# Optimization experiments

Measured on AMD Instinct MI355X. Metric: run time of the kernel, lower is better.

The kernel has to match this reference:

```python
import jax, jax.numpy as jnp
import numpy as np

B, P, F, D = 1024, 128, 512, 256
THETA = 1e-7  # numerical-stability constant (ratio-model denominator)


def setup_inputs() -> dict:
    key = jax.random.key(0)
    k1, k2, k3 = jax.random.split(key, 3)
    # xavier_uniform limits for [P, D] and [F, D] parameter matrices
    lim_p = float(np.sqrt(6.0 / (P + D)))
    lim_f = float(np.sqrt(6.0 / (F + D)))
    return {
        "x": jax.random.normal(k1, (B, D), dtype=jnp.float32),
        "prototypes": jax.random.uniform(k2, (P, D), jnp.float32, -lim_p, lim_p),
        "feature_bank": jax.random.uniform(k3, (F, D), jnp.float32, -lim_f, lim_f),
        "alpha": jnp.float32(0.5),
        "beta": jnp.float32(0.5),
    }


def reference(x, prototypes, feature_bank, alpha, beta):
    # Feature memberships: an object 'has' feature w iff <obj, w> > 0.
    xf = x @ feature_bank.T            # [B, F]
    pf = prototypes @ feature_bank.T   # [P, F]
    # Intersection, 'product' reduction: sum_k x_k * p_k over features both have.
    # x_k * 1[x_k>0] = relu(x_k), so this is a single GEMM of the relu'd memberships.
    inter = jnp.einsum("bf,pf->bp", jax.nn.relu(xf), jax.nn.relu(pf))  # [B, P]
    # Differences, 'substractmatch' reduction: over features both objects have,
    # sum of how much more membership one side has than the other.
    both = (xf > 0)[:, None, :] & (pf > 0)[None, :, :]   # [B, P, F]
    diff = xf[:, None, :] - pf[None, :, :]               # [B, P, F]
    zero = jnp.zeros((), dtype=xf.dtype)
    x_minus_p = jnp.sum(jnp.where(both & (diff > 0), diff, zero), axis=-1)   # [B, P]
    p_minus_x = jnp.sum(jnp.where(both & (diff < 0), -diff, zero), axis=-1)  # [B, P]
    # Tversky ratio-model similarity with theta for numerical stability.
    return inter / (inter + alpha * x_minus_p + beta * p_minus_x + THETA)
```

## Files before the change

kernel.cpp:

```cpp
#include <hip/hip_runtime.h>

#define Bn 1024
#define Pn 128
#define Fn 512
#define Dn 256
#define THETA 1e-7f

typedef _Float16 f16;
typedef f16 f16x8 __attribute__((ext_vector_type(8)));
typedef f16 f16x4 __attribute__((ext_vector_type(4)));
typedef f16 f16x2 __attribute__((ext_vector_type(2)));
typedef float f32x4 __attribute__((ext_vector_type(4)));

#if defined(__has_builtin)
#if __has_builtin(__builtin_amdgcn_fdot2)
#define FDOT2(a, b, c) __builtin_amdgcn_fdot2((a), (b), (c), false)
#endif
#endif
#ifndef FDOT2
#define FDOT2(a, b, c) ((float)(a)[0] * (float)(b)[0] + (float)(a)[1] * (float)(b)[1] + (c))
#endif

__device__ __forceinline__ f16x2 get2(const f16x8 v, int idx) {
    union { f16x8 v8; f16x2 v2[4]; } u;
    u.v8 = v;
    return u.v2[idx];
}

__global__ __launch_bounds__(256)
void gemm_feat(const float* __restrict__ x, const float* __restrict__ prot,
               const float* __restrict__ fb,
               f16* __restrict__ RX, f16* __restrict__ BX,
               f16* __restrict__ RPT8, f16* __restrict__ BPT8)
{
    __shared__ float As[64][68];
    __shared__ float Fs[64][68];
    const int tid = threadIdx.x;
    const int rb  = blockIdx.y * 64;
    const int cb  = blockIdx.x * 64;
    const int tx  = tid & 15;
    const int ty  = tid >> 4;
    const int lr  = tid >> 2;
    const int lk  = tid & 3;

    float acc[4][4] = {};

    for (int k0 = 0; k0 < Dn; k0 += 64) {
        #pragma unroll
        for (int q = 0; q < 4; ++q) {
            const int kk = lk + q * 4;
            const int r  = rb + lr;
            const float* asrc = (r < Bn) ? (x + (size_t)r * Dn)
                                         : (prot + (size_t)(r - Bn) * Dn);
            float4 av = *(const float4*)(asrc + k0 + kk * 4);
            float4 fv = *(const float4*)(fb + (size_t)(cb + lr) * Dn + k0 + kk * 4);
            As[kk*4+0][lr] = av.x; As[kk*4+1][lr] = av.y;
            As[kk*4+2][lr] = av.z; As[kk*4+3][lr] = av.w;
            Fs[kk*4+0][lr] = fv.x; Fs[kk*4+1][lr] = fv.y;
            Fs[kk*4+2][lr] = fv.z; Fs[kk*4+3][lr] = fv.w;
        }
        __syncthreads();
        #pragma unroll 8
        for (int k = 0; k < 64; ++k) {
            float4 a = *(const float4*)&As[k][ty * 4];
            float4 f = *(const float4*)&Fs[k][tx * 4];
            const float aa[4] = {a.x, a.y, a.z, a.w};
            const float ff[4] = {f.x, f.y, f.z, f.w};
            #pragma unroll
            for (int i = 0; i < 4; ++i)
                #pragma unroll
                for (int j = 0; j < 4; ++j)
                    acc[i][j] = fmaf(aa[i], ff[j], acc[i][j]);
        }
        __syncthreads();
    }

    #pragma unroll
    for (int i = 0; i < 4; ++i) {
        const int r = rb + ty * 4 + i;
        if (r < Bn) {
            f16x4 rv, bv;
            #pragma unroll
            for (int j = 0; j < 4; ++j) {
                const float v = acc[i][j];
                rv[j] = (f16)fmaxf(v, 0.f);
                bv[j] = (v > 0.f) ? (f16)1 : (f16)0;
            }
            const size_t off = (size_t)r * Fn + cb + tx * 4;
            *(f16x4*)(RX + off) = rv;
            *(f16x4*)(BX + off) = bv;
        } else {
            const int p = r - Bn;
            #pragma unroll
            for (int j = 0; j < 4; ++j) {
                const int c = cb + tx * 4 + j;
                const float v = acc[i][j];
                const size_t off = (size_t)(c >> 3) * (Pn * 8) + p * 8 + (c & 7);
                RPT8[off] = (f16)fmaxf(v, 0.f);
                BPT8[off] = (v > 0.f) ? (f16)1 : (f16)0;
            }
        }
    }
}

__global__ __launch_bounds__(256)
void tversky_main(const f16* __restrict__ RX, const f16* __restrict__ BX,
                  const f16* __restrict__ RPT8, const f16* __restrict__ BPT8,
                  const float* __restrict__ alpha_p, const float* __restrict__ beta_p,
                  float* __restrict__ out)
{
    __shared__ f32x4 sAcc[16][128];
    const int tid   = threadIdx.x;
    const int ot    = tid & 15;
    const int slice = tid >> 4;
    const int bt    = ot >> 1;
    const int pt    = ot & 1;
    const int bb    = blockIdx.x * 16;
    const int pb    = blockIdx.y * 8;
    const int b0    = bb + bt * 2;
    const int p0    = pb + pt * 4;
    const int g0    = slice * 4;

    const f16* xrow0 = RX + (size_t)b0 * Fn;
    const f16* bxr0  = BX + (size_t)b0 * Fn;

    float aI[2][4] = {};
    float aM[2][4] = {};
    float aX[2][4] = {};
    float aP[2][4] = {};
    const f16x2 one2 = {(f16)1, (f16)1};

    #pragma unroll
    for (int g = 0; g < 4; ++g) {
        const size_t xoff = (size_t)(g0 + g) * 8;
        const f16x8 rx0 = *(const f16x8*)(xrow0 + xoff);
        const f16x8 rx1 = *(const f16x8*)(xrow0 + Fn + xoff);
        const f16x8 bx0 = *(const f16x8*)(bxr0 + xoff);
        const f16x8 bx1 = *(const f16x8*)(bxr0 + Fn + xoff);
        const size_t pbase = (size_t)(g0 + g) * (Pn * 8) + (size_t)p0 * 8;
        #pragma unroll
        for (int q = 0; q < 4; ++q) {
            const f16x8 rp = *(const f16x8*)(RPT8 + pbase + q * 8);
            const f16x8 bp = *(const f16x8*)(BPT8 + pbase + q * 8);
            const f16x8 mn0 = __builtin_elementwise_min(rx0, rp);
            const f16x8 mn1 = __builtin_elementwise_min(rx1, rp);
            #pragma unroll
            for (int h = 0; h < 4; ++h) {
                const f16x2 rp2 = get2(rp, h);
                const f16x2 bp2 = get2(bp, h);
                aI[0][q] = FDOT2(get2(rx0, h), rp2,  aI[0][q]);
                aI[1][q] = FDOT2(get2(rx1, h), rp2,  aI[1][q]);
                aM[0][q] = FDOT2(get2(mn0, h), one2, aM[0][q]);
                aM[1][q] = FDOT2(get2(mn1, h), one2, aM[1][q]);
                aX[0][q] = FDOT2(get2(rx0, h), bp2,  aX[0][q]);
                aX[1][q] = FDOT2(get2(rx1, h), bp2,  aX[1][q]);
                aP[0][q] = FDOT2(get2(bx0, h), rp2,  aP[0][q]);
                aP[1][q] = FDOT2(get2(bx1, h), rp2,  aP[1][q]);
            }
        }
    }

    #pragma unroll
    for (int i = 0; i < 2; ++i) {
        #pragma unroll
        for (int q = 0; q < 4; ++q) {
            const int outIdx = (bt * 2 + i) * 8 + pt * 4 + q;
            f32x4 v = {aI[i][q], aM[i][q], aX[i][q], aP[i][q]};
            sAcc[slice][outIdx] = v;
        }
    }
    __syncthreads();

    if (tid < 128) {
        f32x4 acc = sAcc[0][tid];
        #pragma unroll
        for (int s = 1; s < 16; ++s) acc += sAcc[s][tid];
        const float alpha = *alpha_p;
        const float beta  = *beta_p;
        const float I = acc[0], M = acc[1], X = acc[2], P = acc[3];
        const float W = alpha * (X - M) + beta * (P - M);
        const int brow = tid >> 3, pcol = tid & 7;
        out[(size_t)(bb + brow) * Pn + pb + pcol] = I / (I + W + THETA);
    }
}

extern "C" void kernel_launch(void* const* d_in, const int* in_sizes, int n_in,
                              void* d_out, int out_size, void* d_ws, size_t ws_size,
                              hipStream_t stream)
{
    const float* x     = (const float*)d_in[0];
    const float* prot  = (const float*)d_in[1];
    const float* fb    = (const float*)d_in[2];
    const float* alpha = (const float*)d_in[3];
    const float* beta  = (const float*)d_in[4];
    float* out = (float*)d_out;

    f16* RX   = (f16*)d_ws;
    f16* BX   = RX + (size_t)Bn * Fn;
    f16* RPT8 = BX + (size_t)Bn * Fn;
    f16* BPT8 = RPT8 + (size_t)Fn * Pn;

    dim3 gg(Fn / 64, (Bn + Pn) / 64);
    gemm_feat<<<gg, 256, 0, stream>>>(x, prot, fb, RX, BX, RPT8, BPT8);

    dim3 gm(Bn / 16, Pn / 8);
    tversky_main<<<gm, 256, 0, stream>>>(RX, BX, RPT8, BPT8, alpha, beta, out);
}
```

Baseline: 27.29 us.

## Derive binary memberships on the fly and enlarge register tile to 4x4

Stops writing and reading the separate binary membership arrays. Each is rebuilt in registers by clamping small positive relu values to the fp16 minimum normal and computing min(r*65504, 1). The per-thread output tile grows from 2x4 to 4x4 (block tile 16x16), so each loaded RP vector is reused across more batch rows and the grid halves. This cuts global traffic, but adds registers and doubles LDS use for the reduction, which may lower occupancy. The clamp also slightly changes tiny relu values.

Result: no change. 27.66 us (+1.3%).

```diff
diff --git a/kernel.cpp b/kernel.cpp
--- a/kernel.cpp
+++ b/kernel.cpp
@@ -5,6 +5,7 @@
 #define Fn 512
 #define Dn 256
 #define THETA 1e-7f
+#define F16_MINN 6.103515625e-5f
 
 typedef _Float16 f16;
 typedef f16 f16x8 __attribute__((ext_vector_type(8)));
@@ -30,8 +31,7 @@
 __global__ __launch_bounds__(256)
 void gemm_feat(const float* __restrict__ x, const float* __restrict__ prot,
                const float* __restrict__ fb,
-               f16* __restrict__ RX, f16* __restrict__ BX,
-               f16* __restrict__ RPT8, f16* __restrict__ BPT8)
+               f16* __restrict__ RX, f16* __restrict__ RPT8)
 {
     __shared__ float As[64][68];
     __shared__ float Fs[64][68];
@@ -75,103 +75,105 @@
         __syncthreads();
     }
 
+    const f16 MINN = (f16)F16_MINN;
     #pragma unroll
     for (int i = 0; i < 4; ++i) {
         const int r = rb + ty * 4 + i;
         if (r < Bn) {
-            f16x4 rv, bv;
+            f16x4 rv;
             #pragma unroll
             for (int j = 0; j < 4; ++j) {
                 const float v = acc[i][j];
-                rv[j] = (f16)fmaxf(v, 0.f);
-                bv[j] = (v > 0.f) ? (f16)1 : (f16)0;
+                f16 t = (f16)0;
+                if (v > 0.f) { t = (f16)v; if (t < MINN) t = MINN; }
+                rv[j] = t;
             }
-            const size_t off = (size_t)r * Fn + cb + tx * 4;
-            *(f16x4*)(RX + off) = rv;
-            *(f16x4*)(BX + off) = bv;
+            *(f16x4*)(RX + (size_t)r * Fn + cb + tx * 4) = rv;
         } else {
             const int p = r - Bn;
             #pragma unroll
             for (int j = 0; j < 4; ++j) {
                 const int c = cb + tx * 4 + j;
                 const float v = acc[i][j];
-                const size_t off = (size_t)(c >> 3) * (Pn * 8) + p * 8 + (c & 7);
-                RPT8[off] = (f16)fmaxf(v, 0.f);
-                BPT8[off] = (v > 0.f) ? (f16)1 : (f16)0;
+                f16 t = (f16)0;
+                if (v > 0.f) { t = (f16)v; if (t < MINN) t = MINN; }
+                RPT8[(size_t)(c >> 3) * (Pn * 8) + p * 8 + (c & 7)] = t;
             }
         }
     }
 }
 
 __global__ __launch_bounds__(256)
-void tversky_main(const f16* __restrict__ RX, const f16* __restrict__ BX,
-                  const f16* __restrict__ RPT8, const f16* __restrict__ BPT8,
+void tversky_main(const f16* __restrict__ RX, const f16* __restrict__ RPT8,
                   const float* __restrict__ alpha_p, const float* __restrict__ beta_p,
                   float* __restrict__ out)
 {
-    __shared__ f32x4 sAcc[16][128];
+    __shared__ f32x4 sAcc[16][256];
     const int tid   = threadIdx.x;
     const int ot    = tid & 15;
     const int slice = tid >> 4;
-    const int bt    = ot >> 1;
-    const int pt    = ot & 1;
+    const int bt    = ot >> 2;
+    const int pt    = ot & 3;
     const int bb    = blockIdx.x * 16;
-    const int pb    = blockIdx.y * 8;
-    const int b0    = bb + bt * 2;
+    const int pb    = blockIdx.y * 16;
+    const int b0    = bb + bt * 4;
     const int p0    = pb + pt * 4;
     const int g0    = slice * 4;
 
-    const f16* xrow0 = RX + (size_t)b0 * Fn;
-    const f16* bxr0  = BX + (size_t)b0 * Fn;
-
-    float aI[2][4] = {};
-    float aM[2][4] = {};
-    float aX[2][4] = {};
-    float aP[2][4] = {};
+    float aI[4][4] = {};
+    float aM[4][4] = {};
+    float aX[4][4] = {};
+    float aP[4][4] = {};
+
     const f16x2 one2 = {(f16)1, (f16)1};
+    f16x8 KS, ONE8;
+    #pragma unroll
+    for (int e = 0; e < 8; ++e) { KS[e] = (f16)65504.0f; ONE8[e] = (f16)1; }
 
     #pragma unroll
     for (int g = 0; g < 4; ++g) {
         const size_t xoff = (size_t)(g0 + g) * 8;
-        const f16x8 rx0 = *(const f16x8*)(xrow0 + xoff);
-        const f16x8 rx1 = *(const f16x8*)(xrow0 + Fn + xoff);
-        const f16x8 bx0 = *(const f16x8*)(bxr0 + xoff);
-        const f16x8 bx1 = *(const f16x8*)(bxr0 + Fn + xoff);
+        f16x8 rx[4], bx[4];
+        #pragma unroll
+        for (int i = 0; i < 4; ++i) {
+            rx[i] = *(const f16x8*)(RX + (size_t)(b0 + i) * Fn + xoff);
+            bx[i] = __builtin_elementwise_min(rx[i] * KS, ONE8);
+        }
         const size_t pbase = (size_t)(g0 + g) * (Pn * 8) + (size_t)p0 * 8;
+        f16x8 rp[4], bp[4];
         #pragma unroll
         for (int q = 0; q < 4; ++q) {
-            const f16x8 rp = *(const f16x8*)(RPT8 + pbase + q * 8);
-            const f16x8 bp = *(const f16x8*)(BPT8 + pbase + q * 8);
-            const f16x8 mn0 = __builtin_elementwise_min(rx0, rp);
-            const f16x8 mn1 = __builtin_elementwise_min(rx1, rp);
-            #pragma unroll
-            for (int h = 0; h < 4; ++h) {
-                const f16x2 rp2 = get2(rp, h);
-                const f16x2 bp2 = get2(bp, h);
-                aI[0][q] = FDOT2(get2(rx0, h), rp2,  aI[0][q]);
-                aI[1][q] = FDOT2(get2(rx1, h), rp2,  aI[1][q]);
-                aM[0][q] = FDOT2(get2(mn0, h), one2, aM[0][q]);
-                aM[1][q] = FDOT2(get2(mn1, h), one2, aM[1][q]);
-                aX[0][q] = FDOT2(get2(rx0, h), bp2,  aX[0][q]);
-                aX[1][q] = FDOT2(get2(rx1, h), bp2,  aX[1][q]);
-                aP[0][q] = FDOT2(get2(bx0, h), rp2,  aP[0][q]);
-                aP[1][q] = FDOT2(get2(bx1, h), rp2,  aP[1][q]);
+            rp[q] = *(const f16x8*)(RPT8 + pbase + q * 8);
+            bp[q] = __builtin_elementwise_min(rp[q] * KS, ONE8);
+        }
+        #pragma unroll
+        for (int i = 0; i < 4; ++i) {
+            #pragma unroll
+            for (int q = 0; q < 4; ++q) {
+                const f16x8 mn = __builtin_elementwise_min(rx[i], rp[q]);
+                #pragma unroll
+                for (int h = 0; h < 4; ++h) {
+                    aI[i][q] = FDOT2(get2(rx[i], h), get2(rp[q], h), aI[i][q]);
+                    aM[i][q] = FDOT2(get2(mn, h),    one2,           aM[i][q]);
+                    aX[i][q] = FDOT2(get2(rx[i], h), get2(bp[q], h), aX[i][q]);
+                    aP[i][q] = FDOT2(get2(bx[i], h), get2(rp[q], h), aP[i][q]);
+                }
             }
         }
     }
 
     #pragma unroll
-    for (int i = 0; i < 2; ++i) {
+    for (int i = 0; i < 4; ++i) {
         #pragma unroll
         for (int q = 0; q < 4; ++q) {
-            const int outIdx = (bt * 2 + i) * 8 + pt * 4 + q;
+            const int outIdx = (bt * 4 + i) * 16 + pt * 4 + q;
             f32x4 v = {aI[i][q], aM[i][q], aX[i][q], aP[i][q]};
             sAcc[slice][outIdx] = v;
         }
     }
     __syncthreads();
 
-    if (tid < 128) {
+    {
         f32x4 acc = sAcc[0][tid];
         #pragma unroll
         for (int s = 1; s < 16; ++s) acc += sAcc[s][tid];
@@ -179,7 +181,7 @@
         const float beta  = *beta_p;
         const float I = acc[0], M = acc[1], X = acc[2], P = acc[3];
         const float W = alpha * (X - M) + beta * (P - M);
-        const int brow = tid >> 3, pcol = tid & 7;
+        const int brow = tid >> 4, pcol = tid & 15;
         out[(size_t)(bb + brow) * Pn + pb + pcol] = I / (I + W + THETA);
     }
 }
@@ -196,13 +198,11 @@
     float* out = (float*)d_out;
 
     f16* RX   = (f16*)d_ws;
-    f16* BX   = RX + (size_t)Bn * Fn;
-    f16* RPT8 = BX + (size_t)Bn * Fn;
-    f16* BPT8 = RPT8 + (size_t)Fn * Pn;
+    f16* RPT8 = RX + (size_t)Bn * Fn;
 
     dim3 gg(Fn / 64, (Bn + Pn) / 64);
-    gemm_feat<<<gg, 256, 0, stream>>>(x, prot, fb, RX, BX, RPT8, BPT8);
-
-    dim3 gm(Bn / 16, Pn / 8);
-    tversky_main<<<gm, 256, 0, stream>>>(RX, BX, RPT8, BPT8, alpha, beta, out);
-}
+    gemm_feat<<<gg, 256, 0, stream>>>(x, prot, fb, RX, RPT8);
+
+    dim3 gm(Bn / 16, Pn / 16);
+    tversky_main<<<gm, 256, 0, stream>>>(RX, RPT8, alpha, beta, out);
+}
```
